# Performance work log

Measured on AMD Instinct MI355X. Metric: run time of the kernel, lower is better.

The kernel has to match this reference:

```python
import jax, jax.numpy as jnp
import numpy as np

COMMITMENT_COST = 0.25
ENTROPY_LOSS_RATIO = 0.1
ENTROPY_TEMPERATURE = 0.01


def setup_inputs() -> dict:
    key = jax.random.key(0)
    k1, k2 = jax.random.split(key)
    x = jax.random.normal(k1, (64, 32, 32, 256), dtype=jnp.float32)
    # variance_scaling(fan_in, uniform) init for the codebook parameter
    codebook_size, emb_dim = 1024, 256
    limit = jnp.sqrt(3.0 / emb_dim)
    codebook = jax.random.uniform(k2, (codebook_size, emb_dim), jnp.float32, -limit, limit)
    return {"x": x, "codebook": codebook}


def _squared_euclidean_distance(a, b):
    # a: (n, d), b: (m, d) -> (n, m)
    a2 = jnp.sum(a * a, axis=1, keepdims=True)          # (n, 1)
    b2 = jnp.sum(b * b, axis=1)[None, :]                # (1, m)
    ab = jnp.matmul(a, b.T)                             # (n, m)
    return a2 - 2.0 * ab + b2


def _entropy_loss(affinity, temperature):
    # affinity: (..., K); loss_type='softmax'
    flat = affinity.reshape(-1, affinity.shape[-1]) / temperature
    probs = jax.nn.softmax(flat, axis=-1)
    log_probs = jax.nn.log_softmax(flat + 1e-05, axis=-1)
    target_probs = probs
    avg_probs = jnp.mean(target_probs, axis=0)
    avg_entropy = -jnp.sum(avg_probs * jnp.log(avg_probs + 1e-05))
    sample_entropy = -jnp.mean(jnp.sum(target_probs * log_probs, axis=-1))
    return sample_entropy - avg_entropy


def reference(x, codebook):
    sg = jax.lax.stop_gradient
    emb_dim = x.shape[-1]
    codebook_size = codebook.shape[0]
    flat_x = x.reshape(-1, emb_dim)                              # (N, d)
    distances = _squared_euclidean_distance(flat_x, codebook)    # (N, K)
    distances = distances.reshape(x.shape[:-1] + (codebook_size,))
    encoding_indices = jnp.argmin(distances, axis=-1)            # (B,H,W) int
    # quantize: onehot @ codebook == gather of codebook rows
    quantized = jnp.take(codebook, encoding_indices, axis=0)     # (B,H,W,d)

    e_latent_loss = jnp.mean((sg(quantized) - x) ** 2) * COMMITMENT_COST
    q_latent_loss = jnp.mean((quantized - sg(x)) ** 2)
    entropy_loss = _entropy_loss(-distances, ENTROPY_TEMPERATURE) * ENTROPY_LOSS_RATIO
    loss = (e_latent_loss + q_latent_loss + entropy_loss).astype(jnp.float32)

    # straight-through estimator
    quantized = x + sg(quantized - x)
    return quantized, loss, encoding_indices
```

## Files before the change

kernel.cpp:

```cpp
#include <hip/hip_runtime.h>
#include <math.h>

#define NROWS 65536
#define DIM   256
#define KCB   1024
#define TM    64
#define NBLK  (NROWS / TM)
#define QOFF  (NROWS * DIM)
#define IDXOFF (QOFF + 1)

#define WS_DMIN 0
#define WS_PLP  1
#define WS_AVGP 4
#define WS_C2   (WS_AVGP + 8 * 1024)
#define WS_CBF  (WS_C2 + 1024)

#define DELTA 0.05f
#define XPITCH 260

typedef __attribute__((ext_vector_type(8))) __bf16 bf16x8;
typedef __attribute__((ext_vector_type(4))) float  f32x4;
typedef __attribute__((ext_vector_type(8))) unsigned short u16x8;

#define EP_REDD 0
#define EP_REDK 512
#define EP_RT1  1024
#define EP_RT2  1536
#define EP_GMIN 2048
#define EP_CNT  2112
#define EP_CAND 2176
#define EP_CEX  3200
#define EP_R1F  4224
#define EP_SP   4288
#define EP_KFIN 4352
#define EP_DFIN 4416
#define EP_AVGP 4480
#define EP_SIZE 5504

__device__ __forceinline__ unsigned short f2bf(float f) {
    unsigned u = __float_as_uint(f);
    u += 0x7fffu + ((u >> 16) & 1u);
    return (unsigned short)(u >> 16);
}

__device__ __forceinline__ bf16x8 cvt8(const float* src) {
    float4 v0 = *(const float4*)src, v1 = *(const float4*)(src + 4);
    u16x8 o;
    o[0] = f2bf(v0.x); o[1] = f2bf(v0.y); o[2] = f2bf(v0.z); o[3] = f2bf(v0.w);
    o[4] = f2bf(v1.x); o[5] = f2bf(v1.y); o[6] = f2bf(v1.z); o[7] = f2bf(v1.w);
    return __builtin_bit_cast(bf16x8, o);
}

__device__ __forceinline__ void gload_lds16(const void* g, void* l) {
    __builtin_amdgcn_global_load_lds(
        (const __attribute__((address_space(1))) unsigned int*)g,
        (__attribute__((address_space(3))) unsigned int*)l, 16, 0, 0);
}

__global__ __launch_bounds__(256) void prep_kernel(const float* __restrict__ cb,
                                                   float* __restrict__ ws) {
    int gid = blockIdx.x * 256 + threadIdx.x;
    if (gid < 4) ws[gid] = 0.f;
    if (gid < 8192) ws[WS_AVGP + gid] = 0.f;

    int k  = gid >> 5;
    int s  = gid & 31;
    int kc = s >> 2;
    int qq = s & 3;

    if (gid < 1024) {
        const float4* row = (const float4*)(cb + (size_t)gid * DIM);
        float ssum = 0.f;
#pragma unroll 8
        for (int i = 0; i < DIM / 4; ++i) {
            float4 v = row[i];
            ssum += v.x * v.x + v.y * v.y + v.z * v.z + v.w * v.w;
        }
        ws[WS_C2 + gid] = ssum;
    }

    int h  = k >> 9;
    int wc = (k >> 6) & 7;
    int ct = (k >> 4) & 3;
    int m  = k & 15;
    int sub = (kc << 1) + h;
    size_t chunk = ((size_t)sub << 11) + (wc << 8) + (ct << 6) + (qq << 4) + m;

    unsigned short* cbf = (unsigned short*)(ws + WS_CBF);
    const float* src = cb + (size_t)k * DIM + (kc << 5) + (qq << 3);
    float4 v0 = *(const float4*)src, v1 = *(const float4*)(src + 4);
    u16x8 o;
    o[0] = f2bf(v0.x); o[1] = f2bf(v0.y); o[2] = f2bf(v0.z); o[3] = f2bf(v0.w);
    o[4] = f2bf(v1.x); o[5] = f2bf(v1.y); o[6] = f2bf(v1.z); o[7] = f2bf(v1.w);
    *(u16x8*)(cbf + chunk * 8) = o;
}

__global__ __launch_bounds__(1024, 4) void vq_main(const float* __restrict__ x,
                                                   const float* __restrict__ cb,
                                                   float* __restrict__ ws,
                                                   float* __restrict__ out) {
    __shared__ float epi[EP_SIZE];
    __shared__ float xs[64 * XPITCH];
    __shared__ u16x8 ldsB[2][2048];

    const int tid  = threadIdx.x;
    const int w    = tid >> 6;
    const int lane = tid & 63;
    const int m    = lane & 15;
    const int q    = lane >> 4;
    const int wc   = w & 7;
    const int rh   = w >> 3;
    const int R0   = blockIdx.x * TM;

    const char* gB = (const char*)(ws + WS_CBF);
    const int fragoff = (wc << 8) + lane;

    bf16x8 ah[2];

    float4 t0 = *((const float4*)(x + (size_t)(R0 + (w << 2) + 0) * DIM) + lane);
    float4 t1 = *((const float4*)(x + (size_t)(R0 + (w << 2) + 1) * DIM) + lane);
    float4 t2 = *((const float4*)(x + (size_t)(R0 + (w << 2) + 2) * DIM) + lane);
    float4 t3 = *((const float4*)(x + (size_t)(R0 + (w << 2) + 3) * DIM) + lane);

    {
        const char* g = gB + (size_t)tid * 16;
        char* l = (char*)&ldsB[0][0] + (w << 10);
        gload_lds16(g, l);
        gload_lds16(g + 16384, l + 16384);
    }

    *((float4*)(xs + ((w << 2) + 0) * XPITCH) + lane) = t0;
    *((float4*)(xs + ((w << 2) + 1) * XPITCH) + lane) = t1;
    *((float4*)(xs + ((w << 2) + 2) * XPITCH) + lane) = t2;
    *((float4*)(xs + ((w << 2) + 3) * XPITCH) + lane) = t3;

    f32x4 acc[2][8];
#pragma unroll
    for (int a = 0; a < 2; ++a)
#pragma unroll
        for (int b = 0; b < 8; ++b) acc[a][b] = (f32x4)0.f;

    __syncthreads();

    const int rbase = rh << 5;
    ah[0] = cvt8(xs + (rbase + m) * XPITCH + (q << 3));
    ah[1] = cvt8(xs + (rbase + 16 + m) * XPITCH + (q << 3));

#pragma unroll
    for (int sub = 0; sub < 16; ++sub) {
        const int cur = sub & 1;
        if (sub < 15) {
            const char* g = gB + (size_t)(sub + 1) * 32768 + (size_t)tid * 16;
            char* l = (char*)&ldsB[cur ^ 1][0] + (w << 10);
            gload_lds16(g, l);
            gload_lds16(g + 16384, l + 16384);
        }
        const u16x8* lbc = &ldsB[cur][fragoff];
        u16x8 f0 = lbc[0], f1 = lbc[64], f2 = lbc[128], f3 = lbc[192];
#pragma unroll
        for (int ct = 0; ct < 4; ++ct) {
            u16x8 fr = (ct == 0) ? f0 : (ct == 1) ? f1 : (ct == 2) ? f2 : f3;
            bf16x8 bh = __builtin_bit_cast(bf16x8, fr);
            int cg = ((sub & 1) << 2) + ct;
            acc[0][cg] = __builtin_amdgcn_mfma_f32_16x16x32_bf16(ah[0], bh, acc[0][cg], 0, 0, 0);
            acc[1][cg] = __builtin_amdgcn_mfma_f32_16x16x32_bf16(ah[1], bh, acc[1][cg], 0, 0, 0);
        }
        if ((sub & 1) == 1 && sub < 15) {
            const int nkc = (sub >> 1) + 1;
            ah[0] = cvt8(xs + (rbase + m) * XPITCH + (nkc << 5) + (q << 3));
            ah[1] = cvt8(xs + (rbase + 16 + m) * XPITCH + (nkc << 5) + (q << 3));
        }
        if (sub < 15) __syncthreads();
    }

    if (tid < 64) ((int*)(epi + EP_CNT))[tid] = 0;
    epi[EP_AVGP + tid] = 0.f;

    float c2v[8];
#pragma unroll
    for (int cg = 0; cg < 8; ++cg) {
        int col = ((cg >> 2) << 9) + (wc << 6) + ((cg & 3) << 4) + m;
        c2v[cg] = ws[WS_C2 + col];
    }
#pragma unroll
    for (int rt = 0; rt < 2; ++rt) {
#pragma unroll
        for (int reg = 0; reg < 4; ++reg) {
            int row = rbase + (rt << 4) + (q << 2) + reg;
            float md = 3.0e38f; int mk = 0;
#pragma unroll
            for (int cg = 0; cg < 8; ++cg) {
                float g = c2v[cg] - 2.0f * acc[rt][cg][reg];
                acc[rt][cg][reg] = g;
                int col = ((cg >> 2) << 9) + (wc << 6) + ((cg & 3) << 4) + m;
                if (g < md) { md = g; mk = col; }
            }
#pragma unroll
            for (int off = 1; off <= 8; off <<= 1) {
                float od = __shfl_xor(md, off, 64);
                int   ok = __shfl_xor(mk, off, 64);
                if (od < md || (od == md && ok < mk)) { md = od; mk = ok; }
            }
            if (m == 0) {
                epi[EP_REDD + (wc << 6) + row] = md;
                ((int*)(epi + EP_REDK))[(wc << 6) + row] = mk;
            }
        }
    }
    __syncthreads();

    if (tid < 64) {
        float gm = 3.0e38f;
#pragma unroll
        for (int g = 0; g < 8; ++g) {
            float d = epi[EP_REDD + (g << 6) + tid];
            if (d < gm) gm = d;
        }
        epi[EP_GMIN + tid] = gm;
    }
    __syncthreads();

    {
        int* cnt  = (int*)(epi + EP_CNT);
        int* cand = (int*)(epi + EP_CAND);
#pragma unroll
        for (int rt = 0; rt < 2; ++rt) {
#pragma unroll
            for (int reg = 0; reg < 4; ++reg) {
                int row = rbase + (rt << 4) + (q << 2) + reg;
                float gm = epi[EP_GMIN + row];
                float t1 = 0.f, t2 = 0.f;
#pragma unroll
                for (int cg = 0; cg < 8; ++cg) {
                    float g = acc[rt][cg][reg];
                    if (g < gm + DELTA) {
                        int col = ((cg >> 2) << 9) + (wc << 6) + ((cg & 3) << 4) + m;
                        int pos = atomicAdd(&cnt[row], 1);
                        if (pos < 16) cand[(row << 4) + pos] = col;
                    }
                    float z = -100.0f * (g - gm);
                    float e = __expf(z);
                    acc[rt][cg][reg] = e;
                    t1 += e;
                    t2 += e * z;
                }
#pragma unroll
                for (int off = 1; off <= 8; off <<= 1) {
                    t1 += __shfl_xor(t1, off, 64);
                    t2 += __shfl_xor(t2, off, 64);
                }
                if (m == 0) {
                    epi[EP_RT1 + (wc << 6) + row] = t1;
                    epi[EP_RT2 + (wc << 6) + row] = t2;
                }
            }
        }
    }
    __syncthreads();

    if (tid < 64) {
        float T1 = 0.f, T2 = 0.f;
#pragma unroll
        for (int g = 0; g < 8; ++g) {
            T1 += epi[EP_RT1 + (g << 6) + tid];
            T2 += epi[EP_RT2 + (g << 6) + tid];
        }
        float r1 = 1.0f / T1;
        epi[EP_R1F + tid] = r1;
        epi[EP_SP + tid]  = T2 * r1 - logf(T1);
    }
    __syncthreads();

    float sv[8];
    {
        float r1v[2][4];
#pragma unroll
        for (int rt = 0; rt < 2; ++rt)
#pragma unroll
            for (int reg = 0; reg < 4; ++reg)
                r1v[rt][reg] = epi[EP_R1F + rbase + (rt << 4) + (q << 2) + reg];
#pragma unroll
        for (int cg = 0; cg < 8; ++cg) {
            float s = 0.f;
#pragma unroll
            for (int rt = 0; rt < 2; ++rt)
#pragma unroll
                for (int reg = 0; reg < 4; ++reg)
                    s += acc[rt][cg][reg] * r1v[rt][reg];
            s += __shfl_xor(s, 16, 64);
            s += __shfl_xor(s, 32, 64);
            sv[cg] = s;
        }
        if (rh == 0 && lane < 16) {
#pragma unroll
            for (int cg = 0; cg < 8; ++cg) {
                int col = ((cg >> 2) << 9) + (wc << 6) + ((cg & 3) << 4) + m;
                epi[EP_AVGP + col] += sv[cg];
            }
        }
    }
    {
        int* cnt  = (int*)(epi + EP_CNT);
        int* cand = (int*)(epi + EP_CAND);
        int r = tid >> 4;
        int i = tid & 15;
        int n = cnt[r]; if (n > 16) n = 16;
        if (i < n) {
            int k = cand[(r << 4) + i];
            const float4* ax = (const float4*)(xs + r * XPITCH);
            const float4* bx = (const float4*)(cb + (((size_t)k) << 8));
            float ab = 0.f, x2 = 0.f;
#pragma unroll 8
            for (int d4 = 0; d4 < 64; ++d4) {
                float4 a = ax[d4], b = bx[d4];
                ab = fmaf(a.x, b.x, ab);
                ab = fmaf(a.y, b.y, ab);
                ab = fmaf(a.z, b.z, ab);
                ab = fmaf(a.w, b.w, ab);
                x2 += a.x * a.x + a.y * a.y + a.z * a.z + a.w * a.w;
            }
            float t = 2.0f * ab;
            epi[EP_CEX + (r << 4) + i] = (x2 - t) + ws[WS_C2 + k];
        }
    }
    __syncthreads();

    if (rh == 1 && lane < 16) {
#pragma unroll
        for (int cg = 0; cg < 8; ++cg) {
            int col = ((cg >> 2) << 9) + (wc << 6) + ((cg & 3) << 4) + m;
            epi[EP_AVGP + col] += sv[cg];
        }
    }

    if (tid < 64) {
        int* cnt  = (int*)(epi + EP_CNT);
        int* cand = (int*)(epi + EP_CAND);
        int n = cnt[tid]; if (n > 16) n = 16;
        float bd = epi[EP_CEX + (tid << 4)];
        int   bk = cand[(tid << 4)];
        for (int i = 1; i < n; ++i) {
            float d = epi[EP_CEX + (tid << 4) + i];
            int   k = cand[(tid << 4) + i];
            if (d < bd || (d == bd && k < bk)) { bd = d; bk = k; }
        }
        ((int*)(epi + EP_KFIN))[tid] = bk;
        epi[EP_DFIN + tid] = bd;
        out[IDXOFF + R0 + tid] = (float)bk;
    }
    __syncthreads();

#pragma unroll
    for (int rr = 0; rr < 4; ++rr) {
        int r = (w << 2) + rr;
        int k = ((int*)(epi + EP_KFIN))[r];
        f32x4 v = *((const f32x4*)(cb + (((size_t)k) << 8)) + lane);
        __builtin_nontemporal_store(v, (f32x4*)(out + (((size_t)(R0 + r)) << 8)) + lane);
    }
    atomicAdd(ws + WS_AVGP + ((blockIdx.x & 7) << 10) + tid, epi[EP_AVGP + tid]);
    if (tid < 64) {
        float sp = epi[EP_SP + tid];
        float dd = epi[EP_DFIN + tid];
#pragma unroll
        for (int off = 1; off <= 32; off <<= 1) {
            sp += __shfl_xor(sp, off, 64);
            dd += __shfl_xor(dd, off, 64);
        }
        if (tid == 0) {
            atomicAdd(ws + WS_PLP, sp);
            atomicAdd(ws + WS_DMIN, dd);
        }
    }
}

__global__ __launch_bounds__(256) void vq_finalize(const float* __restrict__ ws,
                                                   float* __restrict__ out) {
    __shared__ float red[4];
    int tid = threadIdx.x;
    float part = 0.f;
    for (int k = tid; k < 1024; k += 256) {
        float s = 0.f;
#pragma unroll
        for (int r = 0; r < 8; ++r) s += ws[WS_AVGP + (r << 10) + k];
        float ap = s * (1.0f / 65536.0f);
        part += ap * logf(ap + 1e-5f);
    }
#pragma unroll
    for (int off = 32; off; off >>= 1) part += __shfl_xor(part, off, 64);
    if ((tid & 63) == 0) red[tid >> 6] = part;
    __syncthreads();
    if (tid == 0) {
        float sum_aplog      = red[0] + red[1] + red[2] + red[3];
        float avg_entropy    = -sum_aplog;
        float sample_entropy = -ws[WS_PLP] * (1.0f / 65536.0f);
        float entropy_loss   = (sample_entropy - avg_entropy) * 0.1f;
        float eq = 1.25f * ws[WS_DMIN] * (1.0f / ((float)NROWS * (float)DIM));
        out[QOFF] = eq + entropy_loss;
    }
}

extern "C" void kernel_launch(void* const* d_in, const int* in_sizes, int n_in,
                              void* d_out, int out_size, void* d_ws, size_t ws_size,
                              hipStream_t stream) {
    const float* x  = (const float*)d_in[0];
    const float* cb = (const float*)d_in[1];
    float* out = (float*)d_out;
    float* ws  = (float*)d_ws;

    prep_kernel<<<128, 256, 0, stream>>>(cb, ws);
    vq_main<<<NBLK, 1024, 0, stream>>>(x, cb, ws, out);
    vq_finalize<<<1, 256, 0, stream>>>(ws, out);
}
```

Baseline: 250.5 us.

## Deepen codebook LDS pipeline to 4 stages and fold finalize into main kernel

Restructures the MFMA main loop into 32 half-size stages in a 4-deep LDS ring, with 3 loads in flight. Each half of the waves computes on alternate stages, and the loop uses explicit vmcnt waits, s_setprio and sched barriers in place of a full syncthreads per stage. The epilogue scratch now aliases the B ring buffer, which cuts LDS use and may raise occupancy. The separate finalize kernel is removed: a last-block atomic counter does the final entropy reduction, saving one launch. The counter in the workspace must be zeroed beforehand, presumably by prep_kernel, and each wave now idles on alternate stages.

```diff
diff --git a/kernel.cpp b/kernel.cpp
--- a/kernel.cpp
+++ b/kernel.cpp
@@ -11,6 +11,7 @@
 
 #define WS_DMIN 0
 #define WS_PLP  1
+#define WS_CTR  2
 #define WS_AVGP 4
 #define WS_C2   (WS_AVGP + 8 * 1024)
 #define WS_CBF  (WS_C2 + 1024)
@@ -35,7 +36,6 @@
 #define EP_KFIN 4352
 #define EP_DFIN 4416
 #define EP_AVGP 4480
-#define EP_SIZE 5504
 
 __device__ __forceinline__ unsigned short f2bf(float f) {
     unsigned u = __float_as_uint(f);
@@ -99,9 +99,9 @@
                                                    const float* __restrict__ cb,
                                                    float* __restrict__ ws,
                                                    float* __restrict__ out) {
-    __shared__ float epi[EP_SIZE];
     __shared__ float xs[64 * XPITCH];
-    __shared__ u16x8 ldsB[2][2048];
+    __shared__ u16x8 ldsB[4][1024];
+    float* const epi = (float*)&ldsB[0][0];
 
     const int tid  = threadIdx.x;
     const int w    = tid >> 6;
@@ -113,21 +113,18 @@
     const int R0   = blockIdx.x * TM;
 
     const char* gB = (const char*)(ws + WS_CBF);
-    const int fragoff = (wc << 8) + lane;
-
-    bf16x8 ah[2];
 
     float4 t0 = *((const float4*)(x + (size_t)(R0 + (w << 2) + 0) * DIM) + lane);
     float4 t1 = *((const float4*)(x + (size_t)(R0 + (w << 2) + 1) * DIM) + lane);
     float4 t2 = *((const float4*)(x + (size_t)(R0 + (w << 2) + 2) * DIM) + lane);
     float4 t3 = *((const float4*)(x + (size_t)(R0 + (w << 2) + 3) * DIM) + lane);
 
-    {
-        const char* g = gB + (size_t)tid * 16;
-        char* l = (char*)&ldsB[0][0] + (w << 10);
-        gload_lds16(g, l);
-        gload_lds16(g + 16384, l + 16384);
-    }
+#define STAGE(gr) do {                                                      \
+        const char* g_ = gB + ((size_t)(gr) << 14) + (size_t)tid * 16;      \
+        char* l_ = (char*)&ldsB[(gr) & 3][0] + (w << 10);                   \
+        gload_lds16(g_, l_);                                                \
+    } while (0)
+    STAGE(0); STAGE(1); STAGE(2);
 
     *((float4*)(xs + ((w << 2) + 0) * XPITCH) + lane) = t0;
     *((float4*)(xs + ((w << 2) + 1) * XPITCH) + lane) = t1;
@@ -143,35 +140,46 @@
     __syncthreads();
 
     const int rbase = rh << 5;
+    bf16x8 ah[2];
     ah[0] = cvt8(xs + (rbase + m) * XPITCH + (q << 3));
     ah[1] = cvt8(xs + (rbase + 16 + m) * XPITCH + (q << 3));
 
-#pragma unroll
-    for (int sub = 0; sub < 16; ++sub) {
-        const int cur = sub & 1;
-        if (sub < 15) {
-            const char* g = gB + (size_t)(sub + 1) * 32768 + (size_t)tid * 16;
-            char* l = (char*)&ldsB[cur ^ 1][0] + (w << 10);
-            gload_lds16(g, l);
-            gload_lds16(g + 16384, l + 16384);
-        }
-        const u16x8* lbc = &ldsB[cur][fragoff];
-        u16x8 f0 = lbc[0], f1 = lbc[64], f2 = lbc[128], f3 = lbc[192];
-#pragma unroll
-        for (int ct = 0; ct < 4; ++ct) {
-            u16x8 fr = (ct == 0) ? f0 : (ct == 1) ? f1 : (ct == 2) ? f2 : f3;
-            bf16x8 bh = __builtin_bit_cast(bf16x8, fr);
-            int cg = ((sub & 1) << 2) + ct;
-            acc[0][cg] = __builtin_amdgcn_mfma_f32_16x16x32_bf16(ah[0], bh, acc[0][cg], 0, 0, 0);
-            acc[1][cg] = __builtin_amdgcn_mfma_f32_16x16x32_bf16(ah[1], bh, acc[1][cg], 0, 0, 0);
-        }
-        if ((sub & 1) == 1 && sub < 15) {
-            const int nkc = (sub >> 1) + 1;
+    const int myhalf = wc >> 2;
+    const int fragbuf = ((wc & 3) << 8) + lane;
+
+#pragma unroll
+    for (int g = 0; g < 32; ++g) {
+        if (g + 3 < 32) STAGE(g + 3);
+        if (myhalf == (g & 1)) {
+            const u16x8* lbc = &ldsB[g & 3][fragbuf];
+            u16x8 f0 = lbc[0], f1 = lbc[64], f2 = lbc[128], f3 = lbc[192];
+            __builtin_amdgcn_s_setprio(1);
+#pragma unroll
+            for (int ct = 0; ct < 4; ++ct) {
+                u16x8 fr = (ct == 0) ? f0 : (ct == 1) ? f1 : (ct == 2) ? f2 : f3;
+                bf16x8 bh = __builtin_bit_cast(bf16x8, fr);
+                int cg = (((g >> 1) & 1) << 2) + ct;
+                acc[0][cg] = __builtin_amdgcn_mfma_f32_16x16x32_bf16(ah[0], bh, acc[0][cg], 0, 0, 0);
+                acc[1][cg] = __builtin_amdgcn_mfma_f32_16x16x32_bf16(ah[1], bh, acc[1][cg], 0, 0, 0);
+            }
+            __builtin_amdgcn_s_setprio(0);
+        }
+        if ((g & 3) == 3 && g < 31) {
+            const int nkc = (g >> 2) + 1;
             ah[0] = cvt8(xs + (rbase + m) * XPITCH + (nkc << 5) + (q << 3));
             ah[1] = cvt8(xs + (rbase + 16 + m) * XPITCH + (nkc << 5) + (q << 3));
         }
-        if (sub < 15) __syncthreads();
-    }
+        if (g < 31) {
+            __builtin_amdgcn_sched_barrier(0);
+            if (g < 29)       asm volatile("s_waitcnt vmcnt(2)" ::: "memory");
+            else if (g == 29) asm volatile("s_waitcnt vmcnt(1)" ::: "memory");
+            else              asm volatile("s_waitcnt vmcnt(0)" ::: "memory");
+            __builtin_amdgcn_sched_barrier(0);
+            __builtin_amdgcn_s_barrier();
+            __builtin_amdgcn_sched_barrier(0);
+        }
+    }
+#undef STAGE
 
     if (tid < 64) ((int*)(epi + EP_CNT))[tid] = 0;
     epi[EP_AVGP + tid] = 0.f;
@@ -371,31 +379,33 @@
             atomicAdd(ws + WS_DMIN, dd);
         }
     }
-}
-
-__global__ __launch_bounds__(256) void vq_finalize(const float* __restrict__ ws,
-                                                   float* __restrict__ out) {
-    __shared__ float red[4];
-    int tid = threadIdx.x;
-    float part = 0.f;
-    for (int k = tid; k < 1024; k += 256) {
+
+    __threadfence();
+    __syncthreads();
+    if (tid == 0) {
+        unsigned old = atomicAdd((unsigned int*)(ws + WS_CTR), 1u);
+        ((int*)xs)[0] = (old == (unsigned)(NBLK - 1)) ? 1 : 0;
+    }
+    __syncthreads();
+    if (((int*)xs)[0]) {
         float s = 0.f;
 #pragma unroll
-        for (int r = 0; r < 8; ++r) s += ws[WS_AVGP + (r << 10) + k];
+        for (int r = 0; r < 8; ++r) s += atomicAdd(ws + WS_AVGP + (r << 10) + tid, 0.f);
         float ap = s * (1.0f / 65536.0f);
-        part += ap * logf(ap + 1e-5f);
-    }
-#pragma unroll
-    for (int off = 32; off; off >>= 1) part += __shfl_xor(part, off, 64);
-    if ((tid & 63) == 0) red[tid >> 6] = part;
-    __syncthreads();
-    if (tid == 0) {
-        float sum_aplog      = red[0] + red[1] + red[2] + red[3];
-        float avg_entropy    = -sum_aplog;
-        float sample_entropy = -ws[WS_PLP] * (1.0f / 65536.0f);
-        float entropy_loss   = (sample_entropy - avg_entropy) * 0.1f;
-        float eq = 1.25f * ws[WS_DMIN] * (1.0f / ((float)NROWS * (float)DIM));
-        out[QOFF] = eq + entropy_loss;
+        float part = ap * logf(ap + 1e-5f);
+#pragma unroll
+        for (int off = 1; off <= 32; off <<= 1) part += __shfl_xor(part, off, 64);
+        if (lane == 0) epi[w] = part;
+        __syncthreads();
+        if (tid == 0) {
+            float sum_aplog = 0.f;
+            for (int i = 0; i < 16; ++i) sum_aplog += epi[i];
+            float avg_entropy    = -sum_aplog;
+            float sample_entropy = -atomicAdd(ws + WS_PLP, 0.f) * (1.0f / 65536.0f);
+            float entropy_loss   = (sample_entropy - avg_entropy) * 0.1f;
+            float eq = 1.25f * atomicAdd(ws + WS_DMIN, 0.f) * (1.0f / ((float)NROWS * (float)DIM));
+            out[QOFF] = eq + entropy_loss;
+        }
     }
 }
 
@@ -409,5 +419,4 @@
 
     prep_kernel<<<128, 256, 0, stream>>>(cb, ws);
     vq_main<<<NBLK, 1024, 0, stream>>>(x, cb, ws, out);
-    vq_finalize<<<1, 256, 0, stream>>>(ws, out);
-}
+}
```

Measured after the change: 653.7 us. 161% more time.
